# Kernel optimization log

Hardware: AMD Instinct MI355X
Metric: run time of the kernel (lower is better)

The kernel has to match this reference:

```python
import jax, jax.numpy as jnp
import numpy as np

HEADS = 16  # init kwarg heads

def setup_inputs() -> dict:
    key = jax.random.key(0)
    kx, kq, kk, kv = jax.random.split(key, 4)
    B, C, H, W = 8, 256, 128, 128
    c_out = 256
    s = 1.0 / np.sqrt(C)
    return {
        "x": jax.random.normal(kx, (B, C, H, W), dtype=jnp.float32),
        "wq": jax.random.normal(kq, (c_out, C), dtype=jnp.float32) * s,
        "wk": jax.random.normal(kk, (c_out, C), dtype=jnp.float32) * s,
        "wv": jax.random.normal(kv, (c_out, C), dtype=jnp.float32) * s,
    }

def _feature_map(t):
    return jax.nn.elu(t) + 1.0

def reference(x, wq, wk, wv):
    B, C, H, W = x.shape
    M = H * W
    c_out = wq.shape[0]
    dh = c_out // HEADS
    # 1x1 conv (no bias) == channel matmul; reshape to [B, heads, dh, M]
    def proj(w):
        return jnp.einsum('bchw,oc->bohw', x, w).reshape(B, HEADS, dh, M)
    q = _feature_map(proj(wq))
    k = _feature_map(proj(wk))
    v = proj(wv)
    # original: kv = einsum('bhdk,bhdm->bhkm', k, v); out = einsum('bhdk,bhkm->bhdm', q, kv)
    # reassociated (identical math, avoids [M,M] intermediate):
    A = jnp.einsum('bhdm,bhem->bhde', q, k)          # [B,h,dh,dh]
    out = jnp.einsum('bhde,bhem->bhdm', A, v)         # [B,h,dh,M]
    # z = 1/(einsum('bhdk,bhdm->bhm', q, k.sum(-1, keepdims=True)) + 1e-6) -> [B,h,1]
    z = 1.0 / (jnp.einsum('bhdm,bhd->bh', q, k.sum(-1)) + 1e-6)
    # torch: out * z.unsqueeze(1) with z [B,h,1] -> [B,1,h,1]; requires dh == heads
    out = out * z[:, None, :, None]
    return out.reshape(B, HEADS * dh, H, W)
```

## Files before the change

### kernel.cpp

```cpp
#include <hip/hip_runtime.h>

typedef unsigned short ushortT;
typedef unsigned int uintT;
typedef __attribute__((ext_vector_type(8))) short s8v;
typedef __attribute__((ext_vector_type(4))) float f4v;

#define MFMA16(a,b,c) __builtin_amdgcn_mfma_f32_16x16x32_bf16(a,b,c,0,0,0)
#define MTOT 16384
#define XT_STRIDE 264
#define XT_BATCH (16384 * 264)
#define XB32_SH 8448
#define XB32_B  16896

#define GLL(g, l, sz) __builtin_amdgcn_global_load_lds( \
    (const __attribute__((address_space(1))) void*)(g), \
    (__attribute__((address_space(3))) void*)(l), (sz), 0, 0)

#define STAGE32(tt2) do { \
    const char* gb_ = (const char*)(xt + xtb) + (size_t)(tt2) * XB32_B; \
    char* lb_ = (char*)lds + (((tt2) & 1) ? XB32_B : 0); \
    _Pragma("unroll") \
    for (int i_ = 0; i_ < 4; ++i_) GLL(gb_ + i_ * 4096 + t * 16, lb_ + i_ * 4096 + t * 16, 16); \
    if (t < 128) GLL(gb_ + 16384 + t * 4, lb_ + 16384 + t * 4, 4); \
} while (0)

__device__ __forceinline__ ushortT f2bf(float f) {
    uintT u = __float_as_uint(f);
    u += 0x7FFFu + ((u >> 16) & 1u);
    return (ushortT)(u >> 16);
}
__device__ __forceinline__ uintT pack2(float a, float b) {
    return (uintT)f2bf(a) | ((uintT)f2bf(b) << 16);
}
__device__ __forceinline__ float elu1(float p) {
    return p > 0.f ? p + 1.f : __expf(p);
}

__global__ void k_prep(const float* __restrict__ wq, const float* __restrict__ wk,
                       ushortT* __restrict__ wqk, float* __restrict__ accz)
{
    int i = blockIdx.x * 256 + threadIdx.x;
    wqk[i]         = f2bf(wq[i]);
    wqk[65536 + i] = f2bf(wk[i]);
    if (i < 36864) accz[i] = 0.f;
}

__global__ __launch_bounds__(256) void k_tx(const float* __restrict__ x,
                                            ushortT* __restrict__ xt)
{
    __shared__ ushortT tile[64 * 66];
    const int t = threadIdx.x;
    const int m0 = blockIdx.x * 64;
    const int ct = blockIdx.y & 3, b = blockIdx.y >> 2;
    const int c0 = ct * 64;

    const int cl = t >> 4, ml = (t & 15) * 4;
    #pragma unroll
    for (int i = 0; i < 4; ++i) {
        f4v v = *(const f4v*)(x + ((size_t)(b * 256 + c0 + cl + i * 16)) * MTOT + m0 + ml);
        uintT* w = (uintT*)&tile[(cl + i * 16) * 66 + ml];
        w[0] = pack2(v.x, v.y);
        w[1] = pack2(v.z, v.w);
    }
    __syncthreads();
    const int mr = t >> 2, cc = (t & 3) * 16;
    s8v o0, o1;
    #pragma unroll
    for (int u = 0; u < 8; ++u) o0[u] = (short)tile[(cc + u) * 66 + mr];
    #pragma unroll
    for (int u = 0; u < 8; ++u) o1[u] = (short)tile[(cc + 8 + u) * 66 + mr];
    ushortT* dst = xt + (size_t)b * XT_BATCH + (size_t)(m0 + mr) * XT_STRIDE + c0 + cc;
    *(s8v*)dst = o0;
    *(s8v*)(dst + 8) = o1;
}

__global__ __launch_bounds__(256, 2) void k_qk(
    const ushortT* __restrict__ xt, const ushortT* __restrict__ wqk,
    float* __restrict__ Ag, float* __restrict__ qsg, float* __restrict__ ksg)
{
    __shared__ __align__(16) ushortT lds[2 * XB32_SH + 4 * 1280];
    const int t = threadIdx.x;
    const int wv = t >> 6, lane = t & 63, quad = lane >> 4, l15 = lane & 15;
    const int b = blockIdx.y;
    const size_t xtb = (size_t)b * XT_BATCH + (size_t)(blockIdx.x * 256) * XT_STRIDE;

    ushortT* gram = lds + 2 * XB32_SH + wv * 1280;
    float* gramf = (float*)gram;

    f4v accA[4], sQ[4], sK[4];
    #pragma unroll
    for (int i = 0; i < 4; ++i) {
        accA[i] = (f4v){0,0,0,0};
        sQ[i]   = (f4v){0,0,0,0};
        sK[i]   = (f4v){0,0,0,0};
    }
    s8v ones;
    #pragma unroll
    for (int u = 0; u < 8; ++u) ones[u] = (short)0x3F80;

    const ushortT* wq_base = wqk + (wv * 64 + l15) * 256 + quad * 8;
    const ushortT* wk_base = wq_base + 65536;

    STAGE32(0);

    for (int tt = 0; tt < 8; ++tt) {
        __syncthreads();
        if (tt < 7) STAGE32(tt + 1);
        const ushortT* xb = lds + (tt & 1) * XB32_SH;

        f4v aq[4][2], ak[4][2];
        #pragma unroll
        for (int i = 0; i < 4; ++i)
            #pragma unroll
            for (int j = 0; j < 2; ++j) { aq[i][j] = (f4v){0,0,0,0}; ak[i][j] = (f4v){0,0,0,0}; }

        #pragma unroll 2
        for (int kc = 0; kc < 8; ++kc) {
            s8v afq[4], afk[4], bf[2];
            #pragma unroll
            for (int ot = 0; ot < 4; ++ot)
                afq[ot] = *(const s8v*)(wq_base + ot * 16 * 256 + kc * 32);
            #pragma unroll
            for (int ot = 0; ot < 4; ++ot)
                afk[ot] = *(const s8v*)(wk_base + ot * 16 * 256 + kc * 32);
            #pragma unroll
            for (int j = 0; j < 2; ++j)
                bf[j] = *(const s8v*)&xb[(j * 16 + l15) * XT_STRIDE + kc * 32 + quad * 8];
            #pragma unroll
            for (int ot = 0; ot < 4; ++ot)
                #pragma unroll
                for (int j = 0; j < 2; ++j)
                    aq[ot][j] = MFMA16(afq[ot], bf[j], aq[ot][j]);
            #pragma unroll
            for (int ot = 0; ot < 4; ++ot)
                #pragma unroll
                for (int j = 0; j < 2; ++j)
                    ak[ot][j] = MFMA16(afk[ot], bf[j], ak[ot][j]);
        }

        #pragma unroll
        for (int ot = 0; ot < 4; ++ot)
            #pragma unroll
            for (int j = 0; j < 2; ++j)
                #pragma unroll
                for (int r = 0; r < 4; ++r) {
                    aq[ot][j][r] = elu1(aq[ot][j][r]);
                    ak[ot][j][r] = elu1(ak[ot][j][r]);
                }

        #pragma unroll
        for (int ot = 0; ot < 4; ++ot) {
            #pragma unroll
            for (int jj = 0; jj < 2; ++jj)
                #pragma unroll
                for (int r = 0; r < 4; ++r) {
                    int d = quad * 4 + r;
                    gram[d * 40 + jj * 16 + l15]        = f2bf(aq[ot][jj][r]);
                    gram[(16 + d) * 40 + jj * 16 + l15] = f2bf(ak[ot][jj][r]);
                }
            s8v qa = *(const s8v*)&gram[l15 * 40 + quad * 8];
            s8v kb = *(const s8v*)&gram[(16 + l15) * 40 + quad * 8];
            accA[ot] = MFMA16(qa, kb, accA[ot]);
            sQ[ot]   = MFMA16(qa, ones, sQ[ot]);
            sK[ot]   = MFMA16(kb, ones, sK[ot]);
        }
    }

    #pragma unroll
    for (int ot = 0; ot < 4; ++ot)
        #pragma unroll
        for (int r = 0; r < 4; ++r)
            atomicAdd(Ag + ((b * 16 + wv * 4 + ot) * 16 + quad * 4 + r) * 16 + l15, accA[ot][r]);

    if (l15 == 0) {
        #pragma unroll
        for (int ot = 0; ot < 4; ++ot)
            #pragma unroll
            for (int r = 0; r < 4; ++r) {
                int row = ot * 16 + quad * 4 + r;
                gramf[row]      = sQ[ot][r];
                gramf[64 + row] = sK[ot][r];
            }
    }
    float myq = gramf[lane];
    float myk = gramf[64 + lane];
    atomicAdd(qsg + b * 256 + wv * 64 + lane, myq);
    atomicAdd(ksg + b * 256 + wv * 64 + lane, myk);
}

__global__ __launch_bounds__(256) void k_weff(
    const float* __restrict__ wvw, const float* __restrict__ Ag,
    const float* __restrict__ qsg, const float* __restrict__ ksg,
    ushortT* __restrict__ weff)
{
    __shared__ float A_l[256];
    __shared__ float z_l[16];
    const int t = threadIdx.x;
    const int h = blockIdx.x, b = blockIdx.y;
    A_l[t] = Ag[(b * 16 + h) * 256 + t];
    if (t < 16) {
        float s = 0.f;
        #pragma unroll
        for (int d = 0; d < 16; ++d)
            s += qsg[b * 256 + t * 16 + d] * ksg[b * 256 + t * 16 + d];
        z_l[t] = 1.f / (s + 1e-6f);
    }
    __syncthreads();
    float acc[16];
    #pragma unroll
    for (int d = 0; d < 16; ++d) acc[d] = 0.f;
    #pragma unroll 4
    for (int e = 0; e < 16; ++e) {
        float w = wvw[(h * 16 + e) * 256 + t];
        #pragma unroll
        for (int d = 0; d < 16; ++d) acc[d] += A_l[d * 16 + e] * w;
    }
    #pragma unroll
    for (int d = 0; d < 16; ++d)
        weff[((size_t)b * 256 + h * 16 + d) * 256 + t] = f2bf(acc[d] * z_l[d]);
}

__global__ __launch_bounds__(256, 2) void k_out(
    const ushortT* __restrict__ xt, const ushortT* __restrict__ weff,
    float* __restrict__ out)
{
    __shared__ __align__(16) ushortT lds[2 * XB32_SH];
    const int t = threadIdx.x;
    const int wv = t >> 6, lane = t & 63, quad = lane >> 4, l15 = lane & 15;
    const int b = blockIdx.y;
    const size_t xtb = (size_t)b * XT_BATCH + (size_t)(blockIdx.x * 256) * XT_STRIDE;

    const ushortT* w_base = weff + (size_t)b * 65536 + (wv * 64 + l15) * 256 + quad * 8;

    STAGE32(0);

    for (int tt = 0; tt < 8; ++tt) {
        __syncthreads();
        if (tt < 7) STAGE32(tt + 1);
        const ushortT* xb = lds + (tt & 1) * XB32_SH;

        f4v acc[4][2];
        #pragma unroll
        for (int i = 0; i < 4; ++i)
            #pragma unroll
            for (int j = 0; j < 2; ++j) acc[i][j] = (f4v){0,0,0,0};

        #pragma unroll 2
        for (int kc = 0; kc < 8; ++kc) {
            s8v af[4], bf[2];
            #pragma unroll
            for (int ot = 0; ot < 4; ++ot)
                af[ot] = *(const s8v*)(w_base + ot * 16 * 256 + kc * 32);
            #pragma unroll
            for (int j = 0; j < 2; ++j)
                bf[j] = *(const s8v*)&xb[(j * 16 + l15) * XT_STRIDE + kc * 32 + quad * 8];
            #pragma unroll
            for (int ot = 0; ot < 4; ++ot)
                #pragma unroll
                for (int j = 0; j < 2; ++j)
                    acc[ot][j] = MFMA16(af[ot], bf[j], acc[ot][j]);
        }

        const int m0 = blockIdx.x * 256 + tt * 32;
        #pragma unroll
        for (int ot = 0; ot < 4; ++ot)
            #pragma unroll
            for (int j = 0; j < 2; ++j)
                #pragma unroll
                for (int r = 0; r < 4; ++r)
                    out[((size_t)b * 256 + wv * 64 + ot * 16 + quad * 4 + r) * MTOT
                        + m0 + j * 16 + l15] = acc[ot][j][r];
    }
}

extern "C" void kernel_launch(void* const* d_in, const int* in_sizes, int n_in,
                              void* d_out, int out_size, void* d_ws, size_t ws_size,
                              hipStream_t stream)
{
    const float* x   = (const float*)d_in[0];
    const float* wq  = (const float*)d_in[1];
    const float* wk  = (const float*)d_in[2];
    const float* wvw = (const float*)d_in[3];
    float* out = (float*)d_out;
    char* ws = (char*)d_ws;
    ushortT* wqk  = (ushortT*)ws;
    float*   Ag   = (float*)(ws + 262144);
    float*   qsg  = (float*)(ws + 393216);
    float*   ksg  = (float*)(ws + 401408);
    ushortT* weff = (ushortT*)(ws + 409600);
    ushortT* xt   = (ushortT*)(ws + 1458176);

    hipLaunchKernelGGL(k_prep, dim3(256), dim3(256), 0, stream, wq, wk, wqk, Ag);
    hipLaunchKernelGGL(k_tx,   dim3(256, 32), dim3(256), 0, stream, x, xt);
    hipLaunchKernelGGL(k_qk,   dim3(64, 8), dim3(256), 0, stream, xt, wqk, Ag, qsg, ksg);
    hipLaunchKernelGGL(k_weff, dim3(16, 8),  dim3(256), 0, stream, wvw, Ag, qsg, ksg, weff);
    hipLaunchKernelGGL(k_out,  dim3(64, 8), dim3(256), 0, stream, xt, weff, out);
}
```

Baseline: 448.5 us.

## Split k_qk and k_out into 64-pixel blocks with single-shot staging

Each block of the QK-gram and output kernels now handles 64 pixels instead of looping over 256 with double buffering. Each block loads its 64-row tile of transposed x once into LDS and computes a 4x64 MFMA tile. The grid grows fourfold to 2048 blocks, and launch bounds rise to allow more resident blocks per CU. This trades the software pipeline for more parallelism and occupancy, but adds more atomics on A and reloads the weight fragments in every block.

Result: faster. 398.9 us (-11.1%).

```diff
diff --git a/kernel.cpp b/kernel.cpp
--- a/kernel.cpp
+++ b/kernel.cpp
@@ -9,19 +9,19 @@
 #define MTOT 16384
 #define XT_STRIDE 264
 #define XT_BATCH (16384 * 264)
-#define XB32_SH 8448
-#define XB32_B  16896
+#define XB64_SH 16896
+#define XB64_B  33792
 
 #define GLL(g, l, sz) __builtin_amdgcn_global_load_lds( \
     (const __attribute__((address_space(1))) void*)(g), \
     (__attribute__((address_space(3))) void*)(l), (sz), 0, 0)
 
-#define STAGE32(tt2) do { \
-    const char* gb_ = (const char*)(xt + xtb) + (size_t)(tt2) * XB32_B; \
-    char* lb_ = (char*)lds + (((tt2) & 1) ? XB32_B : 0); \
+#define STAGE64() do { \
+    const char* gb_ = (const char*)(xt + xtb); \
+    char* lb_ = (char*)lds; \
     _Pragma("unroll") \
-    for (int i_ = 0; i_ < 4; ++i_) GLL(gb_ + i_ * 4096 + t * 16, lb_ + i_ * 4096 + t * 16, 16); \
-    if (t < 128) GLL(gb_ + 16384 + t * 4, lb_ + 16384 + t * 4, 4); \
+    for (int i_ = 0; i_ < 8; ++i_) GLL(gb_ + i_ * 4096 + t * 16, lb_ + i_ * 4096 + t * 16, 16); \
+    GLL(gb_ + 32768 + t * 4, lb_ + 32768 + t * 4, 4); \
 } while (0)
 
 __device__ __forceinline__ ushortT f2bf(float f) {
@@ -74,17 +74,17 @@
     *(s8v*)(dst + 8) = o1;
 }
 
-__global__ __launch_bounds__(256, 2) void k_qk(
+__global__ __launch_bounds__(256, 3) void k_qk(
     const ushortT* __restrict__ xt, const ushortT* __restrict__ wqk,
     float* __restrict__ Ag, float* __restrict__ qsg, float* __restrict__ ksg)
 {
-    __shared__ __align__(16) ushortT lds[2 * XB32_SH + 4 * 1280];
+    __shared__ __align__(16) ushortT lds[XB64_SH + 4 * 1280];
     const int t = threadIdx.x;
     const int wv = t >> 6, lane = t & 63, quad = lane >> 4, l15 = lane & 15;
     const int b = blockIdx.y;
-    const size_t xtb = (size_t)b * XT_BATCH + (size_t)(blockIdx.x * 256) * XT_STRIDE;
-
-    ushortT* gram = lds + 2 * XB32_SH + wv * 1280;
+    const size_t xtb = (size_t)b * XT_BATCH + (size_t)(blockIdx.x * 64) * XT_STRIDE;
+
+    ushortT* gram = lds + XB64_SH + wv * 1280;
     float* gramf = (float*)gram;
 
     f4v accA[4], sQ[4], sK[4];
@@ -99,70 +99,72 @@
     for (int u = 0; u < 8; ++u) ones[u] = (short)0x3F80;
 
     const ushortT* wq_base = wqk + (wv * 64 + l15) * 256 + quad * 8;
-    const ushortT* wk_base = wq_base + 65536;
-
-    STAGE32(0);
-
-    for (int tt = 0; tt < 8; ++tt) {
-        __syncthreads();
-        if (tt < 7) STAGE32(tt + 1);
-        const ushortT* xb = lds + (tt & 1) * XB32_SH;
-
-        f4v aq[4][2], ak[4][2];
-        #pragma unroll
-        for (int i = 0; i < 4; ++i)
-            #pragma unroll
-            for (int j = 0; j < 2; ++j) { aq[i][j] = (f4v){0,0,0,0}; ak[i][j] = (f4v){0,0,0,0}; }
+
+    STAGE64();
+    __syncthreads();
+    const ushortT* xb = lds;
+
+    #pragma unroll
+    for (int op = 0; op < 2; ++op) {
+        f4v aq[2][4], ak[2][4];
+        #pragma unroll
+        for (int oo = 0; oo < 2; ++oo)
+            #pragma unroll
+            for (int j = 0; j < 4; ++j) { aq[oo][j] = (f4v){0,0,0,0}; ak[oo][j] = (f4v){0,0,0,0}; }
 
         #pragma unroll 2
         for (int kc = 0; kc < 8; ++kc) {
-            s8v afq[4], afk[4], bf[2];
-            #pragma unroll
-            for (int ot = 0; ot < 4; ++ot)
-                afq[ot] = *(const s8v*)(wq_base + ot * 16 * 256 + kc * 32);
-            #pragma unroll
-            for (int ot = 0; ot < 4; ++ot)
-                afk[ot] = *(const s8v*)(wk_base + ot * 16 * 256 + kc * 32);
-            #pragma unroll
-            for (int j = 0; j < 2; ++j)
-                bf[j] = *(const s8v*)&xb[(j * 16 + l15) * XT_STRIDE + kc * 32 + quad * 8];
-            #pragma unroll
-            for (int ot = 0; ot < 4; ++ot)
-                #pragma unroll
-                for (int j = 0; j < 2; ++j)
-                    aq[ot][j] = MFMA16(afq[ot], bf[j], aq[ot][j]);
-            #pragma unroll
-            for (int ot = 0; ot < 4; ++ot)
-                #pragma unroll
-                for (int j = 0; j < 2; ++j)
-                    ak[ot][j] = MFMA16(afk[ot], bf[j], ak[ot][j]);
+            s8v afq[2], afk[2], bfv[4];
+            #pragma unroll
+            for (int oo = 0; oo < 2; ++oo) {
+                const ushortT* wb = wq_base + (op * 2 + oo) * 16 * 256 + kc * 32;
+                afq[oo] = *(const s8v*)wb;
+                afk[oo] = *(const s8v*)(wb + 65536);
+            }
+            #pragma unroll
+            for (int j = 0; j < 4; ++j)
+                bfv[j] = *(const s8v*)&xb[(j * 16 + l15) * XT_STRIDE + kc * 32 + quad * 8];
+            #pragma unroll
+            for (int oo = 0; oo < 2; ++oo)
+                #pragma unroll
+                for (int j = 0; j < 4; ++j)
+                    aq[oo][j] = MFMA16(afq[oo], bfv[j], aq[oo][j]);
+            #pragma unroll
+            for (int oo = 0; oo < 2; ++oo)
+                #pragma unroll
+                for (int j = 0; j < 4; ++j)
+                    ak[oo][j] = MFMA16(afk[oo], bfv[j], ak[oo][j]);
         }
 
         #pragma unroll
-        for (int ot = 0; ot < 4; ++ot)
-            #pragma unroll
-            for (int j = 0; j < 2; ++j)
+        for (int oo = 0; oo < 2; ++oo)
+            #pragma unroll
+            for (int j = 0; j < 4; ++j)
                 #pragma unroll
                 for (int r = 0; r < 4; ++r) {
-                    aq[ot][j][r] = elu1(aq[ot][j][r]);
-                    ak[ot][j][r] = elu1(ak[ot][j][r]);
+                    aq[oo][j][r] = elu1(aq[oo][j][r]);
+                    ak[oo][j][r] = elu1(ak[oo][j][r]);
                 }
 
         #pragma unroll
-        for (int ot = 0; ot < 4; ++ot) {
-            #pragma unroll
-            for (int jj = 0; jj < 2; ++jj)
-                #pragma unroll
-                for (int r = 0; r < 4; ++r) {
-                    int d = quad * 4 + r;
-                    gram[d * 40 + jj * 16 + l15]        = f2bf(aq[ot][jj][r]);
-                    gram[(16 + d) * 40 + jj * 16 + l15] = f2bf(ak[ot][jj][r]);
-                }
-            s8v qa = *(const s8v*)&gram[l15 * 40 + quad * 8];
-            s8v kb = *(const s8v*)&gram[(16 + l15) * 40 + quad * 8];
-            accA[ot] = MFMA16(qa, kb, accA[ot]);
-            sQ[ot]   = MFMA16(qa, ones, sQ[ot]);
-            sK[ot]   = MFMA16(kb, ones, sK[ot]);
+        for (int oo = 0; oo < 2; ++oo) {
+            const int ot = op * 2 + oo;
+            #pragma unroll
+            for (int hf = 0; hf < 2; ++hf) {
+                #pragma unroll
+                for (int jj = 0; jj < 2; ++jj)
+                    #pragma unroll
+                    for (int r = 0; r < 4; ++r) {
+                        int d = quad * 4 + r;
+                        gram[d * 40 + jj * 16 + l15]        = f2bf(aq[oo][hf * 2 + jj][r]);
+                        gram[(16 + d) * 40 + jj * 16 + l15] = f2bf(ak[oo][hf * 2 + jj][r]);
+                    }
+                s8v qa = *(const s8v*)&gram[l15 * 40 + quad * 8];
+                s8v kb = *(const s8v*)&gram[(16 + l15) * 40 + quad * 8];
+                accA[ot] = MFMA16(qa, kb, accA[ot]);
+                sQ[ot]   = MFMA16(qa, ones, sQ[ot]);
+                sK[ot]   = MFMA16(kb, ones, sK[ot]);
+            }
         }
     }
 
@@ -220,57 +222,53 @@
         weff[((size_t)b * 256 + h * 16 + d) * 256 + t] = f2bf(acc[d] * z_l[d]);
 }
 
-__global__ __launch_bounds__(256, 2) void k_out(
+__global__ __launch_bounds__(256, 4) void k_out(
     const ushortT* __restrict__ xt, const ushortT* __restrict__ weff,
     float* __restrict__ out)
 {
-    __shared__ __align__(16) ushortT lds[2 * XB32_SH];
+    __shared__ __align__(16) ushortT lds[XB64_SH];
     const int t = threadIdx.x;
     const int wv = t >> 6, lane = t & 63, quad = lane >> 4, l15 = lane & 15;
     const int b = blockIdx.y;
-    const size_t xtb = (size_t)b * XT_BATCH + (size_t)(blockIdx.x * 256) * XT_STRIDE;
+    const size_t xtb = (size_t)b * XT_BATCH + (size_t)(blockIdx.x * 64) * XT_STRIDE;
 
     const ushortT* w_base = weff + (size_t)b * 65536 + (wv * 64 + l15) * 256 + quad * 8;
 
-    STAGE32(0);
-
-    for (int tt = 0; tt < 8; ++tt) {
-        __syncthreads();
-        if (tt < 7) STAGE32(tt + 1);
-        const ushortT* xb = lds + (tt & 1) * XB32_SH;
-
-        f4v acc[4][2];
-        #pragma unroll
-        for (int i = 0; i < 4; ++i)
-            #pragma unroll
-            for (int j = 0; j < 2; ++j) acc[i][j] = (f4v){0,0,0,0};
-
-        #pragma unroll 2
-        for (int kc = 0; kc < 8; ++kc) {
-            s8v af[4], bf[2];
-            #pragma unroll
-            for (int ot = 0; ot < 4; ++ot)
-                af[ot] = *(const s8v*)(w_base + ot * 16 * 256 + kc * 32);
-            #pragma unroll
-            for (int j = 0; j < 2; ++j)
-                bf[j] = *(const s8v*)&xb[(j * 16 + l15) * XT_STRIDE + kc * 32 + quad * 8];
-            #pragma unroll
-            for (int ot = 0; ot < 4; ++ot)
-                #pragma unroll
-                for (int j = 0; j < 2; ++j)
-                    acc[ot][j] = MFMA16(af[ot], bf[j], acc[ot][j]);
-        }
-
-        const int m0 = blockIdx.x * 256 + tt * 32;
+    STAGE64();
+    __syncthreads();
+    const ushortT* xb = lds;
+
+    f4v acc[4][4];
+    #pragma unroll
+    for (int i = 0; i < 4; ++i)
+        #pragma unroll
+        for (int j = 0; j < 4; ++j) acc[i][j] = (f4v){0,0,0,0};
+
+    #pragma unroll 2
+    for (int kc = 0; kc < 8; ++kc) {
+        s8v af[4], bfv[4];
         #pragma unroll
         for (int ot = 0; ot < 4; ++ot)
-            #pragma unroll
-            for (int j = 0; j < 2; ++j)
-                #pragma unroll
-                for (int r = 0; r < 4; ++r)
-                    out[((size_t)b * 256 + wv * 64 + ot * 16 + quad * 4 + r) * MTOT
-                        + m0 + j * 16 + l15] = acc[ot][j][r];
-    }
+            af[ot] = *(const s8v*)(w_base + ot * 16 * 256 + kc * 32);
+        #pragma unroll
+        for (int j = 0; j < 4; ++j)
+            bfv[j] = *(const s8v*)&xb[(j * 16 + l15) * XT_STRIDE + kc * 32 + quad * 8];
+        #pragma unroll
+        for (int ot = 0; ot < 4; ++ot)
+            #pragma unroll
+            for (int j = 0; j < 4; ++j)
+                acc[ot][j] = MFMA16(af[ot], bfv[j], acc[ot][j]);
+    }
+
+    const int m0 = blockIdx.x * 64;
+    #pragma unroll
+    for (int ot = 0; ot < 4; ++ot)
+        #pragma unroll
+        for (int j = 0; j < 4; ++j)
+            #pragma unroll
+            for (int r = 0; r < 4; ++r)
+                out[((size_t)b * 256 + wv * 64 + ot * 16 + quad * 4 + r) * MTOT
+                    + m0 + j * 16 + l15] = acc[ot][j][r];
 }
 
 extern "C" void kernel_launch(void* const* d_in, const int* in_sizes, int n_in,
@@ -292,7 +290,7 @@
 
     hipLaunchKernelGGL(k_prep, dim3(256), dim3(256), 0, stream, wq, wk, wqk, Ag);
     hipLaunchKernelGGL(k_tx,   dim3(256, 32), dim3(256), 0, stream, x, xt);
-    hipLaunchKernelGGL(k_qk,   dim3(64, 8), dim3(256), 0, stream, xt, wqk, Ag, qsg, ksg);
+    hipLaunchKernelGGL(k_qk,   dim3(256, 8), dim3(256), 0, stream, xt, wqk, Ag, qsg, ksg);
     hipLaunchKernelGGL(k_weff, dim3(16, 8),  dim3(256), 0, stream, wvw, Ag, qsg, ksg, weff);
-    hipLaunchKernelGGL(k_out,  dim3(64, 8), dim3(256), 0, stream, xt, weff, out);
-}
+    hipLaunchKernelGGL(k_out,  dim3(256, 8), dim3(256), 0, stream, xt, weff, out);
+}
```
